# Optimization experiments

Measured on AMD Instinct MI355X. Metric: run time of the kernel, lower is better.

## Reference

```python
import jax, jax.numpy as jnp
import numpy as np

NUM_HEADS = 4
HEAD_DIM = 64
BN_EPS = 1e-5


def setup_inputs() -> dict:
    key = jax.random.key(0)
    ks = jax.random.split(key, 6)
    B, C, H, W = 8, 256, 48, 48
    HD = NUM_HEADS * HEAD_DIM  # 256
    x = jax.random.normal(ks[0], (B, C, H, W), dtype=jnp.float32)
    q_w = jax.random.normal(ks[1], (HD, C), dtype=jnp.float32) * (1.0 / np.sqrt(C))
    k_w = jax.random.normal(ks[2], (HEAD_DIM, C), dtype=jnp.float32) * (1.0 / np.sqrt(C))
    v_w = jax.random.normal(ks[3], (HEAD_DIM, C), dtype=jnp.float32) * (1.0 / np.sqrt(C))
    proj_w = jax.random.normal(ks[4], (C, HD), dtype=jnp.float32) * (1.0 / np.sqrt(HD))
    proj_b = jnp.zeros((C,), dtype=jnp.float32)
    gamma = jnp.ones((C,), dtype=jnp.float32)
    beta = jnp.zeros((C,), dtype=jnp.float32)
    return {"x": x, "q_w": q_w, "k_w": k_w, "v_w": v_w,
            "proj_w": proj_w, "proj_b": proj_b, "gamma": gamma, "beta": beta}


def reference(x, q_w, k_w, v_w, proj_w, proj_b, gamma, beta):
    B, C, H, W = x.shape
    N = H * W
    scale = HEAD_DIM ** -0.5
    xf = x.reshape(B, C, N)  # 1x1 conv == channel matmul
    q = jnp.einsum('oc,bcn->bon', q_w, xf).reshape(B, NUM_HEADS, HEAD_DIM, N)
    k = jnp.einsum('dc,bcn->bdn', k_w, xf)  # shared single KV head (MQA)
    v = jnp.einsum('dc,bcn->bdn', v_w, xf)
    # scores: [B, heads, N, N]
    attn = jnp.einsum('bhdn,bdm->bhnm', q, k) * scale
    attn = jax.nn.softmax(attn, axis=-1)
    out = jnp.einsum('bhnm,bdm->bhdn', attn, v)  # [B, heads, d, N]
    out = out.reshape(B, NUM_HEADS * HEAD_DIM, N)
    out = jnp.einsum('co,bon->bcn', proj_w, out) + proj_b[None, :, None]
    out = out.reshape(B, C, H, W)
    # BatchNorm2d (training-mode batch statistics, biased variance)
    mean = jnp.mean(out, axis=(0, 2, 3), keepdims=True)
    var = jnp.var(out, axis=(0, 2, 3), keepdims=True)
    out = gamma[None, :, None, None] * (out - mean) * jax.lax.rsqrt(var + BN_EPS) + beta[None, :, None, None]
    return out + x
```

## Files before the change

kernel.cpp:

```cpp
#include <hip/hip_runtime.h>
#include <hip/hip_bf16.h>
#include <math.h>

#define BB 8
#define CCH 256
#define NN 2304
#define NH 4
#define HDIM 64
#define QKV_ROWS 384
#define BN_EPS 1e-5f
#define NTILES 36
#define NPART 288
#define SLOG2E 0.18033688011112042f

typedef short bf16x8 __attribute__((ext_vector_type(8)));
typedef short bf16x4 __attribute__((ext_vector_type(4)));
typedef float f32x4 __attribute__((ext_vector_type(4)));

#if __has_builtin(__builtin_amdgcn_exp2f)
#define EXP2(x) __builtin_amdgcn_exp2f(x)
#else
#define EXP2(x) __expf((x) * 0.6931471805599453f)
#endif

#define MFMA32(a, b, c) __builtin_amdgcn_mfma_f32_16x16x32_bf16(a, b, c, 0, 0, 0)

__device__ __forceinline__ unsigned bfpair(float a, float b) {
    __hip_bfloat162 h = __float22bfloat162_rn(make_float2(a, b));
    return *(unsigned*)&h;
}
__device__ __forceinline__ unsigned short f2bf(float f) {
    unsigned u = __float_as_uint(f);
    u = (u + 0x7FFFu + ((u >> 16) & 1u)) >> 16;
    return (unsigned short)u;
}
__device__ __forceinline__ float bf2f(unsigned short s) {
    return __uint_as_float((unsigned)s << 16);
}

__global__ __launch_bounds__(256) void prep_k(
    const float* __restrict__ x,
    const float* __restrict__ qw, const float* __restrict__ kw,
    const float* __restrict__ vw, const float* __restrict__ pw,
    unsigned short* __restrict__ xT, unsigned short* __restrict__ xb,
    unsigned short* __restrict__ Wb, unsigned short* __restrict__ Pb)
{
    const int bid = blockIdx.x;
    const int tid = threadIdx.x;
    if (bid < 1152) {
        __shared__ float sX[64][65];
        const int b  = bid / 144;
        const int rem = bid - b * 144;
        const int nb = (rem >> 2) * 64;
        const int cb = (rem & 3) * 64;

        #pragma unroll
        for (int u = 0; u < 4; ++u) {
            int c  = (tid >> 4) + 16 * u;
            int n4 = (tid & 15) * 4;
            float4 v = *(const float4*)(x + ((size_t)(b * CCH + cb + c)) * NN + nb + n4);
            sX[c][n4+0] = v.x; sX[c][n4+1] = v.y; sX[c][n4+2] = v.z; sX[c][n4+3] = v.w;
        }
        __syncthreads();

        const int n  = tid >> 2;
        const int cg = (tid & 3) * 16;
        unsigned vals[8];
        #pragma unroll
        for (int p = 0; p < 8; ++p)
            vals[p] = bfpair(sX[cg + 2*p][n], sX[cg + 2*p + 1][n]);
        unsigned short* dst = xT + ((size_t)(b * NN + nb + n)) * CCH + cb + cg;
        *(uint4*)dst = make_uint4(vals[0], vals[1], vals[2], vals[3]);
        *(uint4*)(dst + 8) = make_uint4(vals[4], vals[5], vals[6], vals[7]);

        #pragma unroll
        for (int it = 0; it < 2; ++it) {
            int flat = tid + 256 * it;
            int row = flat >> 3;
            int n8  = (flat & 7) * 8;
            unsigned vv[4];
            #pragma unroll
            for (int p = 0; p < 4; ++p)
                vv[p] = bfpair(sX[row][n8 + 2*p], sX[row][n8 + 2*p + 1]);
            *(uint4*)(xb + ((size_t)(b * CCH + cb + row)) * NN + nb + n8) =
                make_uint4(vv[0], vv[1], vv[2], vv[3]);
        }
    } else {
        int idx = (bid - 1152) * 256 + tid;
        if (idx < 98304) {
            int o = idx >> 8, c = idx & 255;
            float v;
            if (o < 256)      v = qw[(size_t)o * CCH + c] * SLOG2E;
            else if (o < 320) v = kw[(size_t)(o - 256) * CCH + c];
            else              v = vw[(size_t)(o - 320) * CCH + c];
            Wb[idx] = f2bf(v);
        } else {
            int j = idx - 98304;
            if (j < 65536) Pb[j] = f2bf(pw[j]);
        }
    }
}

__global__ __launch_bounds__(128) void qkv_mfma_k(
    const unsigned short* __restrict__ Wb, const unsigned short* __restrict__ xT,
    unsigned short* __restrict__ Qt, unsigned short* __restrict__ Kt,
    unsigned short* __restrict__ Vn)
{
    __shared__ unsigned short sE[2][64 * 72];
    const int tid = threadIdx.x;
    const int wave = tid >> 6;
    const int lane = tid & 63;
    const int quad = lane >> 4;
    const int l15  = lane & 15;
    const int b  = blockIdx.x;
    const int nb = blockIdx.y * 64;
    const int mb = blockIdx.z * 128 + wave * 64;

    const unsigned short* Ab = Wb + (size_t)(mb + l15) * CCH + quad * 8;
    const unsigned short* Bb = xT + ((size_t)(b * NN + nb + l15)) * CCH + quad * 8;

    f32x4 C[4][4] = {};
    bf16x8 aA[2][4], bB[2][4];
    #pragma unroll
    for (int i = 0; i < 4; ++i) aA[0][i] = *(const bf16x8*)(Ab + (size_t)(16*i) * CCH);
    #pragma unroll
    for (int j = 0; j < 4; ++j) bB[0][j] = *(const bf16x8*)(Bb + (size_t)(16*j) * CCH);

    #pragma unroll
    for (int kk = 0; kk < 8; ++kk) {
        const int cur = kk & 1;
        if (kk < 7) {
            const int k1 = (kk + 1) * 32;
            #pragma unroll
            for (int i = 0; i < 4; ++i) aA[cur^1][i] = *(const bf16x8*)(Ab + (size_t)(16*i) * CCH + k1);
            #pragma unroll
            for (int j = 0; j < 4; ++j) bB[cur^1][j] = *(const bf16x8*)(Bb + (size_t)(16*j) * CCH + k1);
        }
        #pragma unroll
        for (int i = 0; i < 4; ++i)
            #pragma unroll
            for (int j = 0; j < 4; ++j)
                C[i][j] = MFMA32(aA[cur][i], bB[cur][j], C[i][j]);
    }

    unsigned short* sEw = &sE[wave][0];
    if (mb < 320) {
        #pragma unroll
        for (int i = 0; i < 4; ++i)
            #pragma unroll
            for (int j = 0; j < 4; ++j) {
                unsigned p01 = bfpair(C[i][j][0], C[i][j][1]);
                unsigned p23 = bfpair(C[i][j][2], C[i][j][3]);
                unsigned short* p = sEw + (16*j + l15) * 72 + 16*i + quad*4;
                *(unsigned*)p = p01;
                *(unsigned*)(p + 2) = p23;
            }
        if (mb < 256) {
            #pragma unroll
            for (int it = 0; it < 8; ++it) {
                int flat = lane + 64 * it;
                int row = flat >> 3;
                int o8  = (flat & 7) * 8;
                uint4 v = *(const uint4*)(sEw + row * 72 + o8);
                *(uint4*)(Qt + ((size_t)(b * NN + nb + row)) * CCH + mb + o8) = v;
            }
        } else {
            #pragma unroll
            for (int it = 0; it < 8; ++it) {
                int flat = lane + 64 * it;
                int row = flat >> 3;
                int o8  = (flat & 7) * 8;
                uint4 v = *(const uint4*)(sEw + row * 72 + o8);
                *(uint4*)(Kt + ((size_t)(b * NN + nb + row)) * 64 + o8) = v;
            }
        }
    } else {
        #pragma unroll
        for (int i = 0; i < 4; ++i)
            #pragma unroll
            for (int j = 0; j < 4; ++j) {
                unsigned p01 = bfpair(C[i][j][0], C[i][j][1]);
                unsigned p23 = bfpair(C[i][j][2], C[i][j][3]);
                unsigned short* p = sEw + (16*i + quad*4) * 72 + 16*j + l15;
                p[0]   = (unsigned short)p01;
                p[72]  = (unsigned short)(p01 >> 16);
                p[144] = (unsigned short)p23;
                p[216] = (unsigned short)(p23 >> 16);
            }
        #pragma unroll
        for (int it = 0; it < 8; ++it) {
            int flat = lane + 64 * it;
            int row = flat >> 3;
            int n8  = (flat & 7) * 8;
            uint4 v = *(const uint4*)(sEw + row * 72 + n8);
            *(uint4*)(Vn + ((size_t)(b * 64 + (mb - 320) + row)) * NN + nb + n8) = v;
        }
    }
}

#define ATT_STEP(STEPN, KCUR, KNXT, VPRV, VNXT, BPP, BPN, DOPV)                  \
    {                                                                            \
        __syncthreads();                                                         \
        if ((STEPN) + 1 < NTILES) {                                              \
            *(bf16x8*)(sKV + (KNXT) + kr0 * 64 + kwc)        = pf[0];            \
            *(bf16x8*)(sKV + (KNXT) + (kr0 + 32) * 64 + kwc) = pf[1];            \
            *(bf16x8*)(sKV + (VNXT) + r0 * 64 + vwc)         = pf[2];            \
            *(bf16x8*)(sKV + (VNXT) + (r0 + 32) * 64 + vwc)  = pf[3];            \
        }                                                                        \
        if ((STEPN) + 2 < NTILES) {                                              \
            const int keys0_ = ((STEPN) + 2) * 64;                               \
            pf[0] = *(const bf16x8*)(Kb + (size_t)keys0_ * 64);                  \
            pf[1] = *(const bf16x8*)(Kb + (size_t)(keys0_ + 32) * 64);           \
            pf[2] = *(const bf16x8*)(Vb + keys0_);                               \
            pf[3] = *(const bf16x8*)(Vb + (size_t)32 * NN + keys0_);             \
        }                                                                        \
        if (DOPV) {                                                              \
            _Pragma("unroll")                                                    \
            for (int jd_ = 0; jd_ < 4; ++jd_) {                                  \
                _Pragma("unroll")                                                \
                for (int kt2_ = 0; kt2_ < 2; ++kt2_) {                           \
                    const int row_ = 16 * jd_ + l15;                             \
                    const int ch_ = ((4 * kt2_ + quad) ^ (row_ & 7)) * 8;        \
                    bf16x8 aV_ = *(const bf16x8*)(sKV + (VPRV) + row_ * 64 + ch_);\
                    O[jd_][0] = MFMA32(aV_, BPP[kt2_][0], O[jd_][0]);            \
                    O[jd_][1] = MFMA32(aV_, BPP[kt2_][1], O[jd_][1]);            \
                }                                                                \
            }                                                                    \
            dacc[0] = MFMA32(vone8, BPP[0][0], dacc[0]);                         \
            dacc[1] = MFMA32(vone8, BPP[0][1], dacc[1]);                         \
            dacc[0] = MFMA32(vone8, BPP[1][0], dacc[0]);                         \
            dacc[1] = MFMA32(vone8, BPP[1][1], dacc[1]);                         \
        }                                                                        \
        f32x4 C_[4][2] = {};                                                     \
        _Pragma("unroll")                                                        \
        for (int s_ = 0; s_ < 2; ++s_) {                                         \
            _Pragma("unroll")                                                    \
            for (int kt_ = 0; kt_ < 4; ++kt_) {                                  \
                const int row_ = 16 * kt_ + l15;                                 \
                const int ch_ = ((s_ * 4 + quad) ^ (row_ & 7)) * 8;              \
                bf16x8 aK_ = *(const bf16x8*)(sKV + (KCUR) + row_ * 64 + ch_);   \
                C_[kt_][0] = MFMA32(aK_, bQ[0][s_], C_[kt_][0]);                 \
                C_[kt_][1] = MFMA32(aK_, bQ[1][s_], C_[kt_][1]);                 \
            }                                                                    \
        }                                                                        \
        _Pragma("unroll")                                                        \
        for (int kt2_ = 0; kt2_ < 2; ++kt2_) {                                   \
            _Pragma("unroll")                                                    \
            for (int qt_ = 0; qt_ < 2; ++qt_) {                                  \
                union { unsigned u[4]; bf16x8 v; } xp_;                          \
                const f32x4 c0_ = C_[2 * kt2_][qt_];                             \
                const f32x4 c1_ = C_[2 * kt2_ + 1][qt_];                         \
                xp_.u[0] = bfpair(EXP2(c0_[0]), EXP2(c0_[1]));                   \
                xp_.u[1] = bfpair(EXP2(c0_[2]), EXP2(c0_[3]));                   \
                xp_.u[2] = bfpair(EXP2(c1_[0]), EXP2(c1_[1]));                   \
                xp_.u[3] = bfpair(EXP2(c1_[2]), EXP2(c1_[3]));                   \
                BPN[kt2_][qt_] = xp_.v;                                          \
            }                                                                    \
        }                                                                        \
    }

#define ROTV(x) x = ((x) == 16384) ? 8192 : (x) + 4096

__global__ __launch_bounds__(256, 3) void attn_k(
    const unsigned short* __restrict__ Qt,
    const unsigned short* __restrict__ Kt,
    const unsigned short* __restrict__ Vn,
    unsigned short* __restrict__ Ao)
{
    __shared__ __align__(16) unsigned short sKV[20480];

    const int tid   = threadIdx.x;
    const int wave  = tid >> 6;
    const int lane  = tid & 63;
    const int quad  = lane >> 4;
    const int l15   = lane & 15;
    const int qoff  = wave * 32;
    const int b     = blockIdx.x;
    const int nb    = blockIdx.y * 128;
    const int head  = blockIdx.z;

    const bf16x8 vone8 = {(short)0x3F80, (short)0x3F80, (short)0x3F80, (short)0x3F80,
                          (short)0x3F80, (short)0x3F80, (short)0x3F80, (short)0x3F80};

    bf16x8 bQ[2][2];
    const unsigned short* QtB = Qt + ((size_t)(b * NN + nb + qoff + l15)) * CCH + head * 64 + quad * 8;
    #pragma unroll
    for (int qt = 0; qt < 2; ++qt)
        #pragma unroll
        for (int s = 0; s < 2; ++s)
            bQ[qt][s] = *(const bf16x8*)(QtB + (size_t)(16*qt) * CCH + s * 32);

    const int r0  = tid >> 3;
    const int c8  = (tid & 7) * 8;
    const int kr0 = (r0 & 3) | (((r0 >> 3) & 3) << 2) | (((r0 >> 2) & 1) << 4);
    const int kwc = ((tid & 7) ^ (kr0 & 7)) * 8;
    const int vwc = ((tid & 7) ^ (r0 & 7)) * 8;

    const unsigned short* Kb = Kt + ((size_t)(b * NN + r0)) * 64 + c8;
    const unsigned short* Vb = Vn + ((size_t)(b * 64 + r0)) * NN + c8;

    bf16x8 pf[4];
    pf[0] = *(const bf16x8*)(Kb);
    pf[1] = *(const bf16x8*)(Kb + (size_t)32 * 64);
    pf[2] = *(const bf16x8*)(Vb);
    pf[3] = *(const bf16x8*)(Vb + (size_t)32 * NN);
    *(bf16x8*)(sKV + kr0 * 64 + kwc)               = pf[0];
    *(bf16x8*)(sKV + (kr0 + 32) * 64 + kwc)        = pf[1];
    *(bf16x8*)(sKV + 8192 + r0 * 64 + vwc)         = pf[2];
    *(bf16x8*)(sKV + 8192 + (r0 + 32) * 64 + vwc)  = pf[3];
    pf[0] = *(const bf16x8*)(Kb + (size_t)64 * 64);
    pf[1] = *(const bf16x8*)(Kb + (size_t)96 * 64);
    pf[2] = *(const bf16x8*)(Vb + 64);
    pf[3] = *(const bf16x8*)(Vb + (size_t)32 * NN + 64);

    f32x4 O[4][2] = {};
    f32x4 dacc[2] = {};
    bf16x8 bPe[2][2], bPo[2][2];

    ATT_STEP(0, 0, 4096, 0 , 12288, bPo , bPe, 0);

    int vPrv = 8192;
    int vNxt = 16384;
    for (int sp = 1; sp < 35; sp += 2) {
        ATT_STEP(sp,     4096, 0,    vPrv, vNxt, bPe, bPo, 1);
        ROTV(vPrv); ROTV(vNxt);
        ATT_STEP(sp + 1, 0,    4096, vPrv, vNxt, bPo, bPe, 1);
        ROTV(vPrv); ROTV(vNxt);
    }
    ATT_STEP(35, 4096, 0, vPrv, vNxt, bPe, bPo, 1);
    ROTV(vPrv);

    #pragma unroll
    for (int jd = 0; jd < 4; ++jd)
        #pragma unroll
        for (int kt2 = 0; kt2 < 2; ++kt2) {
            const int row = 16*jd + l15;
            const int ch  = ((4*kt2 + quad) ^ (row & 7)) * 8;
            bf16x8 aV = *(const bf16x8*)(sKV + vPrv + row * 64 + ch);
            O[jd][0] = MFMA32(aV, bPo[kt2][0], O[jd][0]);
            O[jd][1] = MFMA32(aV, bPo[kt2][1], O[jd][1]);
        }
    dacc[0] = MFMA32(vone8, bPo[0][0], dacc[0]);
    dacc[1] = MFMA32(vone8, bPo[0][1], dacc[1]);
    dacc[0] = MFMA32(vone8, bPo[1][0], dacc[0]);
    dacc[1] = MFMA32(vone8, bPo[1][1], dacc[1]);

    __syncthreads();

    float rinv[2];
    rinv[0] = 1.0f / dacc[0][0];
    rinv[1] = 1.0f / dacc[1][0];
    unsigned short* sT = (unsigned short*)sKV;
    #pragma unroll
    for (int qt = 0; qt < 2; ++qt)
        #pragma unroll
        for (int jd = 0; jd < 4; ++jd) {
            unsigned lo = bfpair(O[jd][qt][0] * rinv[qt], O[jd][qt][1] * rinv[qt]);
            unsigned hi = bfpair(O[jd][qt][2] * rinv[qt], O[jd][qt][3] * rinv[qt]);
            *(uint2*)(sT + (qoff + 16*qt + l15) * 72 + 16*jd + quad*4) = make_uint2(lo, hi);
        }
    __syncthreads();

    #pragma unroll
    for (int it = 0; it < 4; ++it) {
        int flat = tid + 256 * it;
        int row  = flat >> 3;
        int cc8  = (flat & 7) * 8;
        uint4 v = *(const uint4*)(sT + row * 72 + cc8);
        *(uint4*)(Ao + ((size_t)(b * NN + nb + row)) * CCH + head * 64 + cc8) = v;
    }
}

__global__ __launch_bounds__(128) void proj_mfma_k(
    const unsigned short* __restrict__ Pb, const unsigned short* __restrict__ Ao,
    const float* __restrict__ pb, unsigned short* __restrict__ projb,
    float* __restrict__ psum, float* __restrict__ psq)
{
    __shared__ unsigned short sE[2][64 * 72];
    const int tid = threadIdx.x;
    const int wave = tid >> 6;
    const int lane = tid & 63;
    const int quad = lane >> 4;
    const int l15  = lane & 15;
    const int b  = blockIdx.x;
    const int nb = blockIdx.y * 64;
    const int mb = blockIdx.z * 128 + wave * 64;
    const int part = b * NTILES + blockIdx.y;

    const unsigned short* Ab = Pb + (size_t)(mb + l15) * CCH + quad * 8;
    const unsigned short* Bb = Ao + ((size_t)(b * NN + nb + l15)) * CCH + quad * 8;

    f32x4 C[4][4] = {};
    bf16x8 aA[2][4], bB[2][4];
    #pragma unroll
    for (int i = 0; i < 4; ++i) aA[0][i] = *(const bf16x8*)(Ab + (size_t)(16*i) * CCH);
    #pragma unroll
    for (int j = 0; j < 4; ++j) bB[0][j] = *(const bf16x8*)(Bb + (size_t)(16*j) * CCH);

    #pragma unroll
    for (int kk = 0; kk < 8; ++kk) {
        const int cur = kk & 1;
        if (kk < 7) {
            const int k1 = (kk + 1) * 32;
            #pragma unroll
            for (int i = 0; i < 4; ++i) aA[cur^1][i] = *(const bf16x8*)(Ab + (size_t)(16*i) * CCH + k1);
            #pragma unroll
            for (int j = 0; j < 4; ++j) bB[cur^1][j] = *(const bf16x8*)(Bb + (size_t)(16*j) * CCH + k1);
        }
        #pragma unroll
        for (int i = 0; i < 4; ++i)
            #pragma unroll
            for (int j = 0; j < 4; ++j)
                C[i][j] = MFMA32(aA[cur][i], bB[cur][j], C[i][j]);
    }

    unsigned short* sEw = &sE[wave][0];
    #pragma unroll
    for (int i = 0; i < 4; ++i) {
        #pragma unroll
        for (int r = 0; r < 4; ++r) {
            const int ch = mb + 16*i + quad*4 + r;
            const float bias = pb[ch];
            float v0 = C[i][0][r] + bias, v1 = C[i][1][r] + bias;
            float v2 = C[i][2][r] + bias, v3 = C[i][3][r] + bias;
            C[i][0][r] = v0; C[i][1][r] = v1; C[i][2][r] = v2; C[i][3][r] = v3;
            float rs = (v0 + v1) + (v2 + v3);
            float rq = (v0*v0 + v1*v1) + (v2*v2 + v3*v3);
            rs += __shfl_xor(rs, 1); rq += __shfl_xor(rq, 1);
            rs += __shfl_xor(rs, 2); rq += __shfl_xor(rq, 2);
            rs += __shfl_xor(rs, 4); rq += __shfl_xor(rq, 4);
            rs += __shfl_xor(rs, 8); rq += __shfl_xor(rq, 8);
            if (l15 == 0) {
                psum[(size_t)ch * NPART + part] = rs;
                psq [(size_t)ch * NPART + part] = rq;
            }
        }
    }

    #pragma unroll
    for (int i = 0; i < 4; ++i)
        #pragma unroll
        for (int j = 0; j < 4; ++j) {
            unsigned p01 = bfpair(C[i][j][0], C[i][j][1]);
            unsigned p23 = bfpair(C[i][j][2], C[i][j][3]);
            unsigned short* p = sEw + (16*i + quad*4) * 72 + 16*j + l15;
            p[0]   = (unsigned short)p01;
            p[72]  = (unsigned short)(p01 >> 16);
            p[144] = (unsigned short)p23;
            p[216] = (unsigned short)(p23 >> 16);
        }
    #pragma unroll
    for (int it = 0; it < 8; ++it) {
        int flat = lane + 64 * it;
        int row = flat >> 3;
        int n8  = (flat & 7) * 8;
        uint4 v = *(const uint4*)(sEw + row * 72 + n8);
        *(uint4*)(projb + ((size_t)(b * CCH + mb + row)) * NN + nb + n8) = v;
    }
}

__global__ __launch_bounds__(256) void bn_apply_k(
    const unsigned short* __restrict__ projb, const unsigned short* __restrict__ xb,
    const float* __restrict__ psum, const float* __restrict__ psq,
    const float* __restrict__ gamma, const float* __restrict__ beta,
    float* __restrict__ out)
{
    const int tid = threadIdx.x;
    const int b = blockIdx.x;
    const int c = blockIdx.y;

    float s = 0.f, q = 0.f;
    for (int k = tid; k < NPART; k += 256) {
        s += psum[(size_t)c * NPART + k];
        q += psq [(size_t)c * NPART + k];
    }
    __shared__ float rs[256], rq[256];
    rs[tid] = s; rq[tid] = q;
    __syncthreads();
    for (int off = 128; off > 0; off >>= 1) {
        if (tid < off) { rs[tid] += rs[tid + off]; rq[tid] += rq[tid + off]; }
        __syncthreads();
    }
    const float inv_n = 1.0f / (float)(BB * NN);
    float mean = rs[0] * inv_n;
    float var  = rq[0] * inv_n - mean * mean;
    float scv = gamma[c] * rsqrtf(var + BN_EPS);
    float shv = beta[c] - mean * scv;

    #pragma unroll
    for (int it = 0; it < 2; ++it) {
        int chunk = tid + 256 * it;
        if (chunk < 288) {
            size_t base = ((size_t)(b * CCH + c)) * NN + chunk * 8;
            uint4 pv = *(const uint4*)(projb + base);
            uint4 xv = *(const uint4*)(xb + base);
            const unsigned short* pp = (const unsigned short*)&pv;
            const unsigned short* xx = (const unsigned short*)&xv;
            float4 r0, r1;
            r0.x = scv * bf2f(pp[0]) + shv + bf2f(xx[0]);
            r0.y = scv * bf2f(pp[1]) + shv + bf2f(xx[1]);
            r0.z = scv * bf2f(pp[2]) + shv + bf2f(xx[2]);
            r0.w = scv * bf2f(pp[3]) + shv + bf2f(xx[3]);
            r1.x = scv * bf2f(pp[4]) + shv + bf2f(xx[4]);
            r1.y = scv * bf2f(pp[5]) + shv + bf2f(xx[5]);
            r1.z = scv * bf2f(pp[6]) + shv + bf2f(xx[6]);
            r1.w = scv * bf2f(pp[7]) + shv + bf2f(xx[7]);
            *(float4*)(out + base) = r0;
            *(float4*)(out + base + 4) = r1;
        }
    }
}

extern "C" void kernel_launch(void* const* d_in, const int* in_sizes, int n_in,
                              void* d_out, int out_size, void* d_ws, size_t ws_size,
                              hipStream_t stream)
{
    const float* x     = (const float*)d_in[0];
    const float* qw    = (const float*)d_in[1];
    const float* kw    = (const float*)d_in[2];
    const float* vw    = (const float*)d_in[3];
    const float* pw    = (const float*)d_in[4];
    const float* pb    = (const float*)d_in[5];
    const float* gamma = (const float*)d_in[6];
    const float* beta  = (const float*)d_in[7];
    float* out = (float*)d_out;

    char* ws = (char*)d_ws;
    unsigned short* xT = (unsigned short*)ws;
    unsigned short* Ao = (unsigned short*)ws;
    unsigned short* Wb = (unsigned short*)(ws + 9437184);
    unsigned short* Pb = (unsigned short*)(ws + 9633792);
    unsigned short* Qt = (unsigned short*)(ws + 9764864);
    unsigned short* Kt = (unsigned short*)(ws + 19202048);
    unsigned short* Vn = (unsigned short*)(ws + 21561344);
    unsigned short* projb = (unsigned short*)(ws + 9764864);
    float* psum  = (float*)(ws + 28639232);
    float* psq   = (float*)(ws + 28934144);
    unsigned short* xb = (unsigned short*)(ws + 29229056);

    prep_k<<<1792, 256, 0, stream>>>(x, qw, kw, vw, pw, xT, xb, Wb, Pb);

    dim3 g1(BB, NN / 64, 3);
    qkv_mfma_k<<<g1, 128, 0, stream>>>(Wb, xT, Qt, Kt, Vn);

    dim3 g2(BB, NN / 128, NH);
    attn_k<<<g2, 256, 0, stream>>>(Qt, Kt, Vn, Ao);

    dim3 g3(BB, NN / 64, 2);
    proj_mfma_k<<<g3, 128, 0, stream>>>(Pb, Ao, pb, projb, psum, psq);

    dim3 g4(BB, CCH);
    bn_apply_k<<<g4, 256, 0, stream>>>(projb, xb, psum, psq, gamma, beta, out);
}
```

Measured before the change: 190.2 us.

## Stagger attention MFMA clusters across waves, drop bf16 x copy, shuffle-reduce BN stats

Inside the attention loop, even waves now run the PV matmul before QK plus exp, while odd waves run it after. The MFMA clusters are wrapped in s_setprio so the matrix and exp work of different waves can overlap. The prep kernel no longer writes a bf16 copy of x. BN-apply instead reads the fp32 x directly, which removes a write but doubles the residual read bytes and adds precision. The BN statistics reduction now uses wave shuffles instead of a shared-memory tree with many barriers.

```diff
diff --git a/kernel.cpp b/kernel.cpp
--- a/kernel.cpp
+++ b/kernel.cpp
@@ -42,7 +42,7 @@
     const float* __restrict__ x,
     const float* __restrict__ qw, const float* __restrict__ kw,
     const float* __restrict__ vw, const float* __restrict__ pw,
-    unsigned short* __restrict__ xT, unsigned short* __restrict__ xb,
+    unsigned short* __restrict__ xT,
     unsigned short* __restrict__ Wb, unsigned short* __restrict__ Pb)
 {
     const int bid = blockIdx.x;
@@ -72,19 +72,6 @@
         unsigned short* dst = xT + ((size_t)(b * NN + nb + n)) * CCH + cb + cg;
         *(uint4*)dst = make_uint4(vals[0], vals[1], vals[2], vals[3]);
         *(uint4*)(dst + 8) = make_uint4(vals[4], vals[5], vals[6], vals[7]);
-
-        #pragma unroll
-        for (int it = 0; it < 2; ++it) {
-            int flat = tid + 256 * it;
-            int row = flat >> 3;
-            int n8  = (flat & 7) * 8;
-            unsigned vv[4];
-            #pragma unroll
-            for (int p = 0; p < 4; ++p)
-                vv[p] = bfpair(sX[row][n8 + 2*p], sX[row][n8 + 2*p + 1]);
-            *(uint4*)(xb + ((size_t)(b * CCH + cb + row)) * NN + nb + n8) =
-                make_uint4(vv[0], vv[1], vv[2], vv[3]);
-        }
     } else {
         int idx = (bid - 1152) * 256 + tid;
         if (idx < 98304) {
@@ -197,6 +184,62 @@
         }
     }
 }
+
+#define PV_CLUSTER(VPRV, BPP)                                                    \
+    {                                                                            \
+        __builtin_amdgcn_s_setprio(1);                                           \
+        _Pragma("unroll")                                                        \
+        for (int jd_ = 0; jd_ < 4; ++jd_) {                                      \
+            _Pragma("unroll")                                                    \
+            for (int kt2_ = 0; kt2_ < 2; ++kt2_) {                               \
+                const int row_ = 16 * jd_ + l15;                                 \
+                const int ch_ = ((4 * kt2_ + quad) ^ (row_ & 7)) * 8;            \
+                bf16x8 aV_ = *(const bf16x8*)(sKV + (VPRV) + row_ * 64 + ch_);   \
+                O[jd_][0] = MFMA32(aV_, BPP[kt2_][0], O[jd_][0]);                \
+                O[jd_][1] = MFMA32(aV_, BPP[kt2_][1], O[jd_][1]);                \
+            }                                                                    \
+        }                                                                        \
+        dacc[0] = MFMA32(vone8, BPP[0][0], dacc[0]);                             \
+        dacc[1] = MFMA32(vone8, BPP[0][1], dacc[1]);                             \
+        dacc[0] = MFMA32(vone8, BPP[1][0], dacc[0]);                             \
+        dacc[1] = MFMA32(vone8, BPP[1][1], dacc[1]);                             \
+        __builtin_amdgcn_s_setprio(0);                                           \
+    }
+
+#define QK_CLUSTER(KCUR, CARR)                                                   \
+    {                                                                            \
+        __builtin_amdgcn_s_setprio(1);                                           \
+        _Pragma("unroll")                                                        \
+        for (int s_ = 0; s_ < 2; ++s_) {                                         \
+            _Pragma("unroll")                                                    \
+            for (int kt_ = 0; kt_ < 4; ++kt_) {                                  \
+                const int row_ = 16 * kt_ + l15;                                 \
+                const int ch_ = ((s_ * 4 + quad) ^ (row_ & 7)) * 8;              \
+                bf16x8 aK_ = *(const bf16x8*)(sKV + (KCUR) + row_ * 64 + ch_);   \
+                CARR[kt_][0] = MFMA32(aK_, bQ[0][s_], CARR[kt_][0]);             \
+                CARR[kt_][1] = MFMA32(aK_, bQ[1][s_], CARR[kt_][1]);             \
+            }                                                                    \
+        }                                                                        \
+        __builtin_amdgcn_s_setprio(0);                                           \
+    }
+
+#define EXP_CLUSTER(CARR, BPN)                                                   \
+    {                                                                            \
+        _Pragma("unroll")                                                        \
+        for (int kt2_ = 0; kt2_ < 2; ++kt2_) {                                   \
+            _Pragma("unroll")                                                    \
+            for (int qt_ = 0; qt_ < 2; ++qt_) {                                  \
+                union { unsigned u[4]; bf16x8 v; } xp_;                          \
+                const f32x4 c0_ = CARR[2 * kt2_][qt_];                           \
+                const f32x4 c1_ = CARR[2 * kt2_ + 1][qt_];                       \
+                xp_.u[0] = bfpair(EXP2(c0_[0]), EXP2(c0_[1]));                   \
+                xp_.u[1] = bfpair(EXP2(c0_[2]), EXP2(c0_[3]));                   \
+                xp_.u[2] = bfpair(EXP2(c1_[0]), EXP2(c1_[1]));                   \
+                xp_.u[3] = bfpair(EXP2(c1_[2]), EXP2(c1_[3]));                   \
+                BPN[kt2_][qt_] = xp_.v;                                          \
+            }                                                                    \
+        }                                                                        \
+    }
 
 #define ATT_STEP(STEPN, KCUR, KNXT, VPRV, VNXT, BPP, BPN, DOPV)                  \
     {                                                                            \
@@ -214,48 +257,15 @@
             pf[2] = *(const bf16x8*)(Vb + keys0_);                               \
             pf[3] = *(const bf16x8*)(Vb + (size_t)32 * NN + keys0_);             \
         }                                                                        \
-        if (DOPV) {                                                              \
-            _Pragma("unroll")                                                    \
-            for (int jd_ = 0; jd_ < 4; ++jd_) {                                  \
-                _Pragma("unroll")                                                \
-                for (int kt2_ = 0; kt2_ < 2; ++kt2_) {                           \
-                    const int row_ = 16 * jd_ + l15;                             \
-                    const int ch_ = ((4 * kt2_ + quad) ^ (row_ & 7)) * 8;        \
-                    bf16x8 aV_ = *(const bf16x8*)(sKV + (VPRV) + row_ * 64 + ch_);\
-                    O[jd_][0] = MFMA32(aV_, BPP[kt2_][0], O[jd_][0]);            \
-                    O[jd_][1] = MFMA32(aV_, BPP[kt2_][1], O[jd_][1]);            \
-                }                                                                \
-            }                                                                    \
-            dacc[0] = MFMA32(vone8, BPP[0][0], dacc[0]);                         \
-            dacc[1] = MFMA32(vone8, BPP[0][1], dacc[1]);                         \
-            dacc[0] = MFMA32(vone8, BPP[1][0], dacc[0]);                         \
-            dacc[1] = MFMA32(vone8, BPP[1][1], dacc[1]);                         \
-        }                                                                        \
         f32x4 C_[4][2] = {};                                                     \
-        _Pragma("unroll")                                                        \
-        for (int s_ = 0; s_ < 2; ++s_) {                                         \
-            _Pragma("unroll")                                                    \
-            for (int kt_ = 0; kt_ < 4; ++kt_) {                                  \
-                const int row_ = 16 * kt_ + l15;                                 \
-                const int ch_ = ((s_ * 4 + quad) ^ (row_ & 7)) * 8;              \
-                bf16x8 aK_ = *(const bf16x8*)(sKV + (KCUR) + row_ * 64 + ch_);   \
-                C_[kt_][0] = MFMA32(aK_, bQ[0][s_], C_[kt_][0]);                 \
-                C_[kt_][1] = MFMA32(aK_, bQ[1][s_], C_[kt_][1]);                 \
-            }                                                                    \
-        }                                                                        \
-        _Pragma("unroll")                                                        \
-        for (int kt2_ = 0; kt2_ < 2; ++kt2_) {                                   \
-            _Pragma("unroll")                                                    \
-            for (int qt_ = 0; qt_ < 2; ++qt_) {                                  \
-                union { unsigned u[4]; bf16x8 v; } xp_;                          \
-                const f32x4 c0_ = C_[2 * kt2_][qt_];                             \
-                const f32x4 c1_ = C_[2 * kt2_ + 1][qt_];                         \
-                xp_.u[0] = bfpair(EXP2(c0_[0]), EXP2(c0_[1]));                   \
-                xp_.u[1] = bfpair(EXP2(c0_[2]), EXP2(c0_[3]));                   \
-                xp_.u[2] = bfpair(EXP2(c1_[0]), EXP2(c1_[1]));                   \
-                xp_.u[3] = bfpair(EXP2(c1_[2]), EXP2(c1_[3]));                   \
-                BPN[kt2_][qt_] = xp_.v;                                          \
-            }                                                                    \
+        if (evenw) {                                                             \
+            if (DOPV) PV_CLUSTER(VPRV, BPP);                                     \
+            QK_CLUSTER(KCUR, C_);                                                \
+            EXP_CLUSTER(C_, BPN);                                                \
+        } else {                                                                 \
+            QK_CLUSTER(KCUR, C_);                                                \
+            EXP_CLUSTER(C_, BPN);                                                \
+            if (DOPV) PV_CLUSTER(VPRV, BPP);                                     \
         }                                                                        \
     }
 
@@ -275,6 +285,7 @@
     const int quad  = lane >> 4;
     const int l15   = lane & 15;
     const int qoff  = wave * 32;
+    const bool evenw = (wave & 1) == 0;
     const int b     = blockIdx.x;
     const int nb    = blockIdx.y * 128;
     const int head  = blockIdx.z;
@@ -330,20 +341,7 @@
     ATT_STEP(35, 4096, 0, vPrv, vNxt, bPe, bPo, 1);
     ROTV(vPrv);
 
-    #pragma unroll
-    for (int jd = 0; jd < 4; ++jd)
-        #pragma unroll
-        for (int kt2 = 0; kt2 < 2; ++kt2) {
-            const int row = 16*jd + l15;
-            const int ch  = ((4*kt2 + quad) ^ (row & 7)) * 8;
-            bf16x8 aV = *(const bf16x8*)(sKV + vPrv + row * 64 + ch);
-            O[jd][0] = MFMA32(aV, bPo[kt2][0], O[jd][0]);
-            O[jd][1] = MFMA32(aV, bPo[kt2][1], O[jd][1]);
-        }
-    dacc[0] = MFMA32(vone8, bPo[0][0], dacc[0]);
-    dacc[1] = MFMA32(vone8, bPo[0][1], dacc[1]);
-    dacc[0] = MFMA32(vone8, bPo[1][0], dacc[0]);
-    dacc[1] = MFMA32(vone8, bPo[1][1], dacc[1]);
+    PV_CLUSTER(vPrv, bPo);
 
     __syncthreads();
 
@@ -460,7 +458,7 @@
 }
 
 __global__ __launch_bounds__(256) void bn_apply_k(
-    const unsigned short* __restrict__ projb, const unsigned short* __restrict__ xb,
+    const unsigned short* __restrict__ projb, const float* __restrict__ x,
     const float* __restrict__ psum, const float* __restrict__ psq,
     const float* __restrict__ gamma, const float* __restrict__ beta,
     float* __restrict__ out)
@@ -474,16 +472,20 @@
         s += psum[(size_t)c * NPART + k];
         q += psq [(size_t)c * NPART + k];
     }
-    __shared__ float rs[256], rq[256];
-    rs[tid] = s; rq[tid] = q;
+    #pragma unroll
+    for (int off = 32; off > 0; off >>= 1) {
+        s += __shfl_xor(s, off);
+        q += __shfl_xor(q, off);
+    }
+    __shared__ float ws[8];
+    if ((tid & 63) == 0) { ws[tid >> 6] = s; ws[4 + (tid >> 6)] = q; }
     __syncthreads();
-    for (int off = 128; off > 0; off >>= 1) {
-        if (tid < off) { rs[tid] += rs[tid + off]; rq[tid] += rq[tid + off]; }
-        __syncthreads();
-    }
+    const float S = (ws[0] + ws[1]) + (ws[2] + ws[3]);
+    const float Q = (ws[4] + ws[5]) + (ws[6] + ws[7]);
+
     const float inv_n = 1.0f / (float)(BB * NN);
-    float mean = rs[0] * inv_n;
-    float var  = rq[0] * inv_n - mean * mean;
+    float mean = S * inv_n;
+    float var  = Q * inv_n - mean * mean;
     float scv = gamma[c] * rsqrtf(var + BN_EPS);
     float shv = beta[c] - mean * scv;
 
@@ -493,18 +495,18 @@
         if (chunk < 288) {
             size_t base = ((size_t)(b * CCH + c)) * NN + chunk * 8;
             uint4 pv = *(const uint4*)(projb + base);
-            uint4 xv = *(const uint4*)(xb + base);
+            float4 xv0 = *(const float4*)(x + base);
+            float4 xv1 = *(const float4*)(x + base + 4);
             const unsigned short* pp = (const unsigned short*)&pv;
-            const unsigned short* xx = (const unsigned short*)&xv;
             float4 r0, r1;
-            r0.x = scv * bf2f(pp[0]) + shv + bf2f(xx[0]);
-            r0.y = scv * bf2f(pp[1]) + shv + bf2f(xx[1]);
-            r0.z = scv * bf2f(pp[2]) + shv + bf2f(xx[2]);
-            r0.w = scv * bf2f(pp[3]) + shv + bf2f(xx[3]);
-            r1.x = scv * bf2f(pp[4]) + shv + bf2f(xx[4]);
-            r1.y = scv * bf2f(pp[5]) + shv + bf2f(xx[5]);
-            r1.z = scv * bf2f(pp[6]) + shv + bf2f(xx[6]);
-            r1.w = scv * bf2f(pp[7]) + shv + bf2f(xx[7]);
+            r0.x = scv * bf2f(pp[0]) + shv + xv0.x;
+            r0.y = scv * bf2f(pp[1]) + shv + xv0.y;
+            r0.z = scv * bf2f(pp[2]) + shv + xv0.z;
+            r0.w = scv * bf2f(pp[3]) + shv + xv0.w;
+            r1.x = scv * bf2f(pp[4]) + shv + xv1.x;
+            r1.y = scv * bf2f(pp[5]) + shv + xv1.y;
+            r1.z = scv * bf2f(pp[6]) + shv + xv1.z;
+            r1.w = scv * bf2f(pp[7]) + shv + xv1.w;
             *(float4*)(out + base) = r0;
             *(float4*)(out + base + 4) = r1;
         }
@@ -536,9 +538,8 @@
     unsigned short* projb = (unsigned short*)(ws + 9764864);
     float* psum  = (float*)(ws + 28639232);
     float* psq   = (float*)(ws + 28934144);
-    unsigned short* xb = (unsigned short*)(ws + 29229056);
-
-    prep_k<<<1792, 256, 0, stream>>>(x, qw, kw, vw, pw, xT, xb, Wb, Pb);
+
+    prep_k<<<1792, 256, 0, stream>>>(x, qw, kw, vw, pw, xT, Wb, Pb);
 
     dim3 g1(BB, NN / 64, 3);
     qkv_mfma_k<<<g1, 128, 0, stream>>>(Wb, xT, Qt, Kt, Vn);
@@ -550,5 +551,5 @@
     proj_mfma_k<<<g3, 128, 0, stream>>>(Pb, Ao, pb, projb, psum, psq);
 
     dim3 g4(BB, CCH);
-    bn_apply_k<<<g4, 256, 0, stream>>>(projb, xb, psum, psq, gamma, beta, out);
-}
+    bn_apply_k<<<g4, 256, 0, stream>>>(projb, x, psum, psq, gamma, beta, out);
+}
```

Measured after the change: 190.0 us. About the same (-0.1%).
